# Kernel optimization log

Hardware: AMD Instinct MI355X
Metric: run time of the kernel (lower is better)

Reference implementation:

```python
import jax, jax.numpy as jnp
import numpy as np

ALPHA = 0.2  # LeakyReLU negative slope
NEG_INF = -9e15


def setup_inputs() -> dict:
    key = jax.random.key(0)
    k1, k2, k3, k4 = jax.random.split(key, 4)
    B, N, F_IN, F_OUT = 2, 4096, 128, 64
    h = jax.random.normal(k1, (B, N, F_IN), dtype=jnp.float32)
    adj = jax.random.randint(k2, (N, N), 0, 2, dtype=jnp.int32)
    W = jax.random.normal(k3, (F_IN, F_OUT), dtype=jnp.float32) * (1.414 / np.sqrt(F_IN))
    a = jax.random.normal(k4, (2 * F_OUT, 1), dtype=jnp.float32) * 0.1
    return {"h": h, "adj": adj, "W": W, "a": a}


def reference(h, adj, W, a):
    # h: (B, N, F_in), adj: (N, N), W: (F_in, F_out), a: (2*F_out, 1)
    Wh = jnp.einsum("bnf,fo->bno", h, W)  # (B, N, F_out)
    F_out = W.shape[1]
    a1 = a[:F_out, 0]   # attends to source node i
    a2 = a[F_out:, 0]   # attends to target node j
    # e_ij = leakyrelu(a1.Wh_i + a2.Wh_j)  -- rank-1 decomposition of the
    # original cat([Wh_i, Wh_j]) @ a, identical math without O(N^2*2F) tensor.
    s1 = Wh @ a1  # (B, N)
    s2 = Wh @ a2  # (B, N)
    e = s1[:, :, None] + s2[:, None, :]  # (B, N, N)
    e = jnp.where(e >= 0, e, ALPHA * e)  # LeakyReLU
    scores = jnp.where(adj[None, :, :] > 0, e, NEG_INF)
    attention = jax.nn.softmax(scores, axis=-1)
    # dropout=0 (eval/deterministic baseline)
    h_prime = jnp.einsum("bij,bjo->bio", attention, Wh)  # (B, N, F_out)
    return jax.nn.elu(h_prime)  # concat=True branch
```

## Files before the change

kernel.cpp:

```cpp
#include <hip/hip_runtime.h>
#include <hip/hip_bf16.h>
#include <math.h>

#define NB 2
#define NN 4096
#define FIN 128
#define FOUT 64
#define LALPHA 0.2f

#define WS_S1    0
#define WS_S2    (NB*NN)
#define WS_WHT   (2*NB*NN)
#define WS_ABITS (WS_WHT + NB*FOUT*NN/2)


typedef __attribute__((ext_vector_type(8))) short short8;
typedef __attribute__((ext_vector_type(4))) float f32x4;

static __device__ inline unsigned int pack2bf(float x, float y) {
    float2 f2; f2.x = x; f2.y = y;
    __hip_bfloat162 pp = __float22bfloat162_rn(f2);
    return *reinterpret_cast<unsigned int*>(&pp);
}

__global__ __launch_bounds__(256) void k1_proj(const float* __restrict__ h,
                                               const float* __restrict__ W,
                                               const float* __restrict__ a,
                                               const int* __restrict__ adj,
                                               float* __restrict__ ws) {
    __shared__ float tbuf[4][68];
    int gid  = blockIdx.x * 256 + threadIdx.x;
    int wid  = gid >> 6;
    int lane = threadIdx.x & 63;
    int w    = threadIdx.x >> 6;

    int prow  = 2 * blockIdx.x + (threadIdx.x >> 7);
    int pword = threadIdx.x & 127;
    const int4* psrc = (const int4*)&adj[(size_t)prow * NN + pword * 32];
    int4 pv[8];
#pragma unroll
    for (int k = 0; k < 8; ++k) pv[k] = psrc[k];

    const float* hrow = h + (size_t)wid * FIN;
    float h0 = hrow[lane];
    float h1 = hrow[64 + lane];
    float acc = 0.f;
#pragma unroll
    for (int f = 0; f < 64; ++f) {
        float hf = __shfl(h0, f);
        acc = fmaf(hf, W[f * FOUT + lane], acc);
    }
#pragma unroll
    for (int f = 0; f < 64; ++f) {
        float hf = __shfl(h1, f);
        acc = fmaf(hf, W[(64 + f) * FOUT + lane], acc);
    }
    tbuf[w][lane] = acc;
    float v1 = acc * a[lane];
    float v2 = acc * a[FOUT + lane];
#pragma unroll
    for (int off = 32; off; off >>= 1) {
        v1 += __shfl_xor(v1, off);
        v2 += __shfl_xor(v2, off);
    }
    if (lane == 0) {
        ws[WS_S1 + wid] = v1 * 1.44269504088896f;
        ws[WS_S2 + wid] = v2 * 1.44269504088896f;
    }

    unsigned int bits = 0;
#pragma unroll
    for (int k = 0; k < 8; ++k) {
        bits |= (pv[k].x != 0 ? 1u : 0u) << (4 * k);
        bits |= (pv[k].y != 0 ? 1u : 0u) << (4 * k + 1);
        bits |= (pv[k].z != 0 ? 1u : 0u) << (4 * k + 2);
        bits |= (pv[k].w != 0 ? 1u : 0u) << (4 * k + 3);
    }
    ((unsigned int*)(ws + WS_ABITS))[(size_t)prow * 128 + pword] = bits;

    __syncthreads();
    if (threadIdx.x < 64) {
        int f = threadIdx.x;
        int wid0 = blockIdx.x * 4;
        int b  = wid0 >> 12;
        int n0 = wid0 & (NN - 1);
        unsigned short* whT = (unsigned short*)(ws + WS_WHT);
        uint2 pk;
        pk.x = pack2bf(tbuf[0][f], tbuf[1][f]);
        pk.y = pack2bf(tbuf[2][f], tbuf[3][f]);
        size_t off = ((size_t)(b * 128 + (n0 >> 5)) * 2048) + f * 32 + (n0 & 31);
        *(uint2*)&whT[off] = pk;
    }
}

__global__ __launch_bounds__(1024, 4) void k3_attn(const float* __restrict__ ws,
                                                   float* __restrict__ out) {
    __shared__ float red[16][2048];
    __shared__ float lred[16][32];
    const int tid  = threadIdx.x;
    const int w    = tid >> 6;
    const int lane = tid & 63;
    const int col  = lane & 15;
    const int quad = lane >> 4;
    const int rt   = blockIdx.x & 127;
    const int b    = blockIdx.x >> 7;
    const int i0   = rt * 32;
    const int jbase = w * 256;

    const float* __restrict__ s1 = ws + WS_S1 + b * NN;
    const float* __restrict__ s2 = ws + WS_S2 + b * NN;
    const unsigned short* __restrict__ whT =
        (const unsigned short*)(ws + WS_WHT) + (size_t)b * FOUT * NN;
    const unsigned int* __restrict__ abits = (const unsigned int*)(ws + WS_ABITS);

    unsigned int mrow[2][8];
#pragma unroll
    for (int g = 0; g < 2; ++g) {
        const int4* mp = (const int4*)&abits[(size_t)(i0 + g * 16 + col) * 128 + w * 8];
        *(int4*)&mrow[g][0] = mp[0];
        *(int4*)&mrow[g][4] = mp[1];
    }

    float s1a[2];
#pragma unroll
    for (int g = 0; g < 2; ++g) s1a[g] = s1[i0 + g * 16 + col];

    f32x4 acc[2][4];
    float lsum[2] = {0.f, 0.f};
#pragma unroll
    for (int g = 0; g < 2; ++g)
#pragma unroll
        for (int nt = 0; nt < 4; ++nt) acc[g][nt] = (f32x4)0.f;

#pragma unroll
    for (int ks = 0; ks < 8; ++ks) {
        const int j8 = jbase + ks * 32 + quad * 8;
        const unsigned short* wb = whT + (size_t)(w * 8 + ks) * 2048;
        short8 bf[4];
#pragma unroll
        for (int nt = 0; nt < 4; ++nt)
            bf[nt] = *(const short8*)&wb[nt * 512 + col * 32 + quad * 8];

        float4 s2lo = *(const float4*)&s2[j8];
        float4 s2hi = *(const float4*)&s2[j8 + 4];
        float sj[8] = {s2lo.x, s2lo.y, s2lo.z, s2lo.w,
                       s2hi.x, s2hi.y, s2hi.z, s2hi.w};
#pragma unroll
        for (int g = 0; g < 2; ++g) {
            const unsigned int mb = (mrow[g][ks] >> (quad * 8)) & 0xffu;
            float p[8];
#pragma unroll
            for (int jj = 0; jj < 8; ++jj) {
                float e = s1a[g] + sj[jj];
                e = fmaxf(e, LALPHA * e);
                float pe = exp2f(e);
                p[jj] = ((mb >> jj) & 1u) ? pe : 0.f;
                lsum[g] += p[jj];
            }
            unsigned int pk[4];
#pragma unroll
            for (int q = 0; q < 4; ++q) pk[q] = pack2bf(p[2 * q], p[2 * q + 1]);
            short8 afrag = *(short8*)pk;
#pragma unroll
            for (int nt = 0; nt < 4; ++nt)
                acc[g][nt] = __builtin_amdgcn_mfma_f32_16x16x32_bf16(
                    afrag, bf[nt], acc[g][nt], 0, 0, 0);
        }
    }

#pragma unroll
    for (int g = 0; g < 2; ++g) {
        float v = lsum[g];
        v += __shfl_xor(v, 16);
        v += __shfl_xor(v, 32);
        if (quad == 0) lred[w][g * 16 + col] = v;
#pragma unroll
        for (int nt = 0; nt < 4; ++nt)
#pragma unroll
            for (int reg = 0; reg < 4; ++reg)
                red[w][g * 1024 + ((nt * 4 + reg) << 6) + lane] = acc[g][nt][reg];
    }
    __syncthreads();

#pragma unroll
    for (int e = 0; e < 2; ++e) {
        int flat = e * 1024 + tid;
        int f    = flat & 63;
        int r32  = flat >> 6;
        int g    = r32 >> 4;
        int r16  = r32 & 15;
        int q2   = r16 >> 2, reg = r16 & 3;
        int c2   = f & 15,   nt  = f >> 4;
        int ln   = q2 * 16 + c2;
        int off  = g * 1024 + ((nt * 4 + reg) << 6) + ln;
        float acv = 0.f, l = 0.f;
#pragma unroll
        for (int ww = 0; ww < 16; ++ww) {
            acv += red[ww][off];
            l   += lred[ww][g * 16 + r16];
        }
        float v = acv / l;
        out[((size_t)(b * NN + i0 + r32) << 6) + f] = v > 0.f ? v : (__expf(v) - 1.f);
    }
}

extern "C" void kernel_launch(void* const* d_in, const int* in_sizes, int n_in,
                              void* d_out, int out_size, void* d_ws, size_t ws_size,
                              hipStream_t stream) {
    const float* h   = (const float*)d_in[0];
    const int*   adj = (const int*)d_in[1];
    const float* W   = (const float*)d_in[2];
    const float* a   = (const float*)d_in[3];
    float* ws  = (float*)d_ws;
    float* out = (float*)d_out;

    hipLaunchKernelGGL(k1_proj, dim3(NB * NN / 4), dim3(256), 0, stream, h, W, a, adj, ws);
    hipLaunchKernelGGL(k3_attn, dim3(256), dim3(1024), 0, stream, ws, out);
}
```

Before: 144.6 us.

## Double-buffer Wh tiles via global_load_lds into reused reduction LDS

Result: faster. 140.0 us (-3.1%).

```diff
diff --git a/kernel.cpp b/kernel.cpp
--- a/kernel.cpp
+++ b/kernel.cpp
@@ -22,6 +22,11 @@
     __hip_bfloat162 pp = __float22bfloat162_rn(f2);
     return *reinterpret_cast<unsigned int*>(&pp);
 }
+
+#define GLL16(gsrc, ldst)                                                        \
+    __builtin_amdgcn_global_load_lds(                                            \
+        (const __attribute__((address_space(1))) void*)(gsrc),                   \
+        (__attribute__((address_space(3))) void*)(ldst), 16, 0, 0)
 
 __global__ __launch_bounds__(256) void k1_proj(const float* __restrict__ h,
                                                const float* __restrict__ W,
@@ -95,7 +100,7 @@
 
 __global__ __launch_bounds__(1024, 4) void k3_attn(const float* __restrict__ ws,
                                                    float* __restrict__ out) {
-    __shared__ float red[16][2048];
+    __shared__ float redbuf[16 * 2048];
     __shared__ float lred[16][32];
     const int tid  = threadIdx.x;
     const int w    = tid >> 6;
@@ -113,6 +118,10 @@
         (const unsigned short*)(ws + WS_WHT) + (size_t)b * FOUT * NN;
     const unsigned int* __restrict__ abits = (const unsigned int*)(ws + WS_ABITS);
 
+    char* slot = (char*)redbuf + w * 8192;
+    const unsigned short* wsrc = whT + (size_t)w * 8 * 2048;
+    const int lsrc = col * 32 + quad * 8;
+
     unsigned int mrow[2][8];
 #pragma unroll
     for (int g = 0; g < 2; ++g) {
@@ -120,10 +129,28 @@
         *(int4*)&mrow[g][0] = mp[0];
         *(int4*)&mrow[g][4] = mp[1];
     }
-
     float s1a[2];
 #pragma unroll
     for (int g = 0; g < 2; ++g) s1a[g] = s1[i0 + g * 16 + col];
+    asm volatile("s_waitcnt vmcnt(0)" ::: "memory");
+
+    float4 s2lo[2], s2hi[2];
+#define LOAD_S2(ks, sl)                                                   \
+    do {                                                                  \
+        s2lo[sl] = *(const float4*)&s2[jbase + (ks) * 32 + quad * 8];     \
+        s2hi[sl] = *(const float4*)&s2[jbase + (ks) * 32 + quad * 8 + 4]; \
+    } while (0)
+#define ISSUE_TILE(ks, sl)                                                \
+    do {                                                                  \
+        const unsigned short* wb_ = wsrc + (size_t)(ks) * 2048;           \
+        GLL16(wb_ + 0 * 512 + lsrc, slot + (sl) * 4096 + 0 * 1024);       \
+        GLL16(wb_ + 1 * 512 + lsrc, slot + (sl) * 4096 + 1 * 1024);       \
+        GLL16(wb_ + 2 * 512 + lsrc, slot + (sl) * 4096 + 2 * 1024);       \
+        GLL16(wb_ + 3 * 512 + lsrc, slot + (sl) * 4096 + 3 * 1024);       \
+    } while (0)
+
+    LOAD_S2(0, 0); ISSUE_TILE(0, 0);
+    LOAD_S2(1, 1); ISSUE_TILE(1, 1);
 
     f32x4 acc[2][4];
     float lsum[2] = {0.f, 0.f};
@@ -134,17 +161,13 @@
 
 #pragma unroll
     for (int ks = 0; ks < 8; ++ks) {
-        const int j8 = jbase + ks * 32 + quad * 8;
-        const unsigned short* wb = whT + (size_t)(w * 8 + ks) * 2048;
-        short8 bf[4];
-#pragma unroll
-        for (int nt = 0; nt < 4; ++nt)
-            bf[nt] = *(const short8*)&wb[nt * 512 + col * 32 + quad * 8];
-
-        float4 s2lo = *(const float4*)&s2[j8];
-        float4 s2hi = *(const float4*)&s2[j8 + 4];
-        float sj[8] = {s2lo.x, s2lo.y, s2lo.z, s2lo.w,
-                       s2hi.x, s2hi.y, s2hi.z, s2hi.w};
+        const int sl = ks & 1;
+        if (ks == 7) asm volatile("s_waitcnt vmcnt(0)" ::: "memory");
+        else         asm volatile("s_waitcnt vmcnt(6)" ::: "memory");
+
+        float sj[8] = {s2lo[sl].x, s2lo[sl].y, s2lo[sl].z, s2lo[sl].w,
+                       s2hi[sl].x, s2hi[sl].y, s2hi[sl].z, s2hi[sl].w};
+        short8 afrag[2];
 #pragma unroll
         for (int g = 0; g < 2; ++g) {
             const unsigned int mb = (mrow[g][ks] >> (quad * 8)) & 0xffu;
@@ -160,14 +183,20 @@
             unsigned int pk[4];
 #pragma unroll
             for (int q = 0; q < 4; ++q) pk[q] = pack2bf(p[2 * q], p[2 * q + 1]);
-            short8 afrag = *(short8*)pk;
-#pragma unroll
-            for (int nt = 0; nt < 4; ++nt)
-                acc[g][nt] = __builtin_amdgcn_mfma_f32_16x16x32_bf16(
-                    afrag, bf[nt], acc[g][nt], 0, 0, 0);
+            afrag[g] = *(short8*)pk;
         }
-    }
-
+#pragma unroll
+        for (int nt = 0; nt < 4; ++nt) {
+            short8 bf = *(const short8*)(slot + sl * 4096 + nt * 1024 + lane * 16);
+            acc[0][nt] = __builtin_amdgcn_mfma_f32_16x16x32_bf16(
+                afrag[0], bf, acc[0][nt], 0, 0, 0);
+            acc[1][nt] = __builtin_amdgcn_mfma_f32_16x16x32_bf16(
+                afrag[1], bf, acc[1][nt], 0, 0, 0);
+        }
+        if (ks < 6) { LOAD_S2(ks + 2, sl); ISSUE_TILE(ks + 2, sl); }
+    }
+
+    float* red_w = redbuf + w * 2048;
 #pragma unroll
     for (int g = 0; g < 2; ++g) {
         float v = lsum[g];
@@ -178,7 +207,7 @@
         for (int nt = 0; nt < 4; ++nt)
 #pragma unroll
             for (int reg = 0; reg < 4; ++reg)
-                red[w][g * 1024 + ((nt * 4 + reg) << 6) + lane] = acc[g][nt][reg];
+                red_w[g * 1024 + ((nt * 4 + reg) << 6) + lane] = acc[g][nt][reg];
     }
     __syncthreads();
 
@@ -196,7 +225,7 @@
         float acv = 0.f, l = 0.f;
 #pragma unroll
         for (int ww = 0; ww < 16; ++ww) {
-            acv += red[ww][off];
+            acv += redbuf[ww * 2048 + off];
             l   += lred[ww][g * 16 + r16];
         }
         float v = acv / l;
```
